# Performance work log

Hardware: AMD Instinct MI355X
Metric: run time of the kernel (lower is better)

The kernel has to match this reference:

```python
import jax, jax.numpy as jnp
import numpy as np

N = 4096
D_MODEL = 512


def setup_inputs() -> dict:
    key = jax.random.key(0)
    ks = jax.random.split(key, 5)
    scale = 1.0 / np.sqrt(D_MODEL)
    return {
        "x": jax.random.normal(ks[0], (N, D_MODEL), dtype=jnp.float32),
        "Wq": jax.random.normal(ks[1], (D_MODEL, D_MODEL), dtype=jnp.float32) * scale,
        "Wk": jax.random.normal(ks[2], (D_MODEL, D_MODEL), dtype=jnp.float32) * scale,
        "Wv": jax.random.normal(ks[3], (D_MODEL, D_MODEL), dtype=jnp.float32) * scale,
        "Ws": jax.random.normal(ks[4], (1, D_MODEL), dtype=jnp.float32) * scale,
    }


def reference(x, Wq, Wk, Wv, Ws):
    # x: [N, d]; torch nn.Linear(bias=False) computes x @ W.T
    Q = x @ Wq.T  # [N, d]
    K = x @ Wk.T  # [N, d]
    V = x @ Wv.T  # [N, d]
    sigma = jnp.clip(x @ Ws.T, 0.001, 1.0)  # [N, 1]

    # prior association: Gaussian kernel over |i - j| with per-row sigma
    pos = jnp.arange(sigma.shape[0], dtype=jnp.float32)
    diff = jnp.abs(pos[:, None] - pos[None, :])  # [N, N]
    gaussian = jnp.exp(-0.5 * (diff / sigma) ** 2) / jnp.sqrt(2.0 * jnp.pi * sigma)
    P = gaussian / (gaussian.sum(axis=1, keepdims=True) + 1e-8)

    scale = jnp.sqrt(jnp.float32(x.shape[-1]))
    S = jax.nn.softmax((Q @ K.T) / scale, axis=-1)  # [N, N]
    Z = S @ V  # [N, d]
    return Z, P, S
```

## Files before the change

kernel.cpp:

```cpp
#include <hip/hip_runtime.h>
#include <math.h>

#define N_TOK 4096
#define DM 512

typedef _Float16 f16x8 __attribute__((ext_vector_type(8)));
typedef _Float16 f16x4 __attribute__((ext_vector_type(4)));
typedef float f32x4 __attribute__((ext_vector_type(4)));

__device__ __forceinline__ void async_ld16(const ushort* g, ushort* l) {
  __builtin_amdgcn_global_load_lds(
      (const __attribute__((address_space(1))) void*)g,
      (__attribute__((address_space(3))) void*)l, 16, 0, 0);
}

__global__ __launch_bounds__(256) void pack_sigma(
    const float* __restrict__ x, const float* __restrict__ Wq,
    const float* __restrict__ Wk, const float* __restrict__ Wv,
    const float* __restrict__ Ws, _Float16* __restrict__ x16,
    _Float16* __restrict__ Wc16, float* __restrict__ sg) {
  const int b = blockIdx.x;
  const int t = threadIdx.x;
  if (b < 2048) {
    int i = b * 1024 + t * 4;
    float4 v = *(const float4*)&x[i];
    f16x4 o;
    o.x = (_Float16)v.x; o.y = (_Float16)v.y;
    o.z = (_Float16)v.z; o.w = (_Float16)v.w;
    *(f16x4*)&x16[i] = o;
    int col = (t * 4) & 511;
    float4 w = *(const float4*)&Ws[col];
    float p = v.x * w.x + v.y * w.y + v.z * w.z + v.w * w.w;
    __shared__ float red[256];
    red[t] = p;
    __syncthreads();
    int lt = t & 127;
    for (int off = 64; off > 0; off >>= 1) {
      if (lt < off) red[t] += red[t + off];
      __syncthreads();
    }
    if (lt == 0) {
      float s = red[t];
      sg[2 * b + (t >> 7)] = fminf(fmaxf(s, 0.001f), 1.0f);
    }
  } else {
    int e = (b - 2048) * 1024 + t * 4;
    const float* src;
    int le = e & (DM * DM - 1);
    if (e < DM * DM) src = Wq + le;
    else if (e < 2 * DM * DM) src = Wk + le;
    else src = Wv + le;
    float4 v = *(const float4*)src;
    f16x4 o;
    o.x = (_Float16)v.x; o.y = (_Float16)v.y;
    o.z = (_Float16)v.z; o.w = (_Float16)v.w;
    *(f16x4*)&Wc16[e] = o;
  }
}

template <int EPI>
__global__ __launch_bounds__(256) void mfma_f16(
    const _Float16* __restrict__ A, int lda, const _Float16* __restrict__ B,
    int ldb, int K, float scale, float* __restrict__ Cf, int ldc,
    _Float16* __restrict__ D0, _Float16* __restrict__ D1,
    _Float16* __restrict__ D2, float* __restrict__ Part) {
  __shared__ _Float16 lds[2 * 128 * 32];
  _Float16* Ah = lds;
  _Float16* Bh = lds + 128 * 32;

  const int t = threadIdx.x;
  const int w = t >> 6, L = t & 63;
  const int wm = (w >> 1) * 64, wn = (w & 1) * 64;
  const int row = L & 15, quad = L >> 4;
  const int bm = blockIdx.y * 128, bn = blockIdx.x * 128;
  const int kbase = blockIdx.z * K;

  f32x4 acc[4][4] = {{}};

  const int c0 = t, c1 = t + 256;
  const int r0 = c0 >> 2, o0 = (c0 & 3) * 8;
  const int r1 = r0 + 64;

  const ushort* ga0 = (const ushort*)(A + (size_t)(bm + r0) * lda + kbase + o0);
  const ushort* ga1 = (const ushort*)(A + (size_t)(bm + r1) * lda + kbase + o0);
  const ushort* gb0 = (const ushort*)(B + (size_t)(bn + r0) * ldb + kbase + o0);
  const ushort* gb1 = (const ushort*)(B + (size_t)(bn + r1) * ldb + kbase + o0);

  for (int k0 = 0; k0 < K; k0 += 32) {
    async_ld16(ga0, (ushort*)(Ah + c0 * 8));
    async_ld16(ga1, (ushort*)(Ah + c1 * 8));
    async_ld16(gb0, (ushort*)(Bh + c0 * 8));
    async_ld16(gb1, (ushort*)(Bh + c1 * 8));
    ga0 += 32; ga1 += 32; gb0 += 32; gb1 += 32;
    __syncthreads();

    f16x8 a0[4], b0[4];
#pragma unroll
    for (int i = 0; i < 4; ++i)
      a0[i] = *(const f16x8*)&Ah[(wm + i * 16 + row) * 32 + quad * 8];
#pragma unroll
    for (int j = 0; j < 4; ++j)
      b0[j] = *(const f16x8*)&Bh[(wn + j * 16 + row) * 32 + quad * 8];
#pragma unroll
    for (int i = 0; i < 4; ++i)
#pragma unroll
      for (int j = 0; j < 4; ++j)
        acc[i][j] = __builtin_amdgcn_mfma_f32_16x16x32_f16(a0[i], b0[j],
                                                           acc[i][j], 0, 0, 0);
    __syncthreads();
  }

  if (EPI == 1) {
    const int region = bn >> 9;
    _Float16* D = (region == 0) ? D0 : ((region == 1) ? D1 : D2);
#pragma unroll
    for (int i = 0; i < 4; ++i)
#pragma unroll
      for (int j = 0; j < 4; ++j)
#pragma unroll
        for (int r = 0; r < 4; ++r) {
          int gr = bm + wm + i * 16 + quad * 4 + r;
          int nn = (bn & 511) + wn + j * 16 + row;
          D[(size_t)gr * 512 + nn] = (_Float16)acc[i][j][r];
        }
  } else if (EPI == 3) {
#pragma unroll
    for (int i = 0; i < 4; ++i)
#pragma unroll
      for (int j = 0; j < 4; ++j)
#pragma unroll
        for (int r = 0; r < 4; ++r) {
          int gr = bm + wm + i * 16 + quad * 4 + r;
          int gc = bn + wn + j * 16 + row;
          D0[(size_t)gr * ldc + gc] = (_Float16)(acc[i][j][r] * scale);
        }
  } else {
    const int z = blockIdx.z;
    float* dst = (z == 0) ? Cf : (Part + (size_t)(z - 1) * 2097152);
#pragma unroll
    for (int i = 0; i < 4; ++i)
#pragma unroll
      for (int j = 0; j < 4; ++j)
#pragma unroll
        for (int r = 0; r < 4; ++r) {
          int gr = bm + wm + i * 16 + quad * 4 + r;
          int gc = bn + wn + j * 16 + row;
          dst[(size_t)gr * ldc + gc] = acc[i][j][r] * scale;
        }
  }
}

__global__ __launch_bounds__(256) void transpose16(
    const _Float16* __restrict__ V16, _Float16* __restrict__ VT) {
  __shared__ _Float16 T[32][34];
  const int t = threadIdx.x;
  const int r = t >> 3, c4 = (t & 7) * 4;
  f16x4 v = *(const f16x4*)&V16[(size_t)(blockIdx.y * 32 + r) * 512 +
                                blockIdx.x * 32 + c4];
  T[r][c4] = v.x; T[r][c4 + 1] = v.y; T[r][c4 + 2] = v.z; T[r][c4 + 3] = v.w;
  __syncthreads();
  f16x4 o;
  o.x = T[c4][r]; o.y = T[c4 + 1][r]; o.z = T[c4 + 2][r]; o.w = T[c4 + 3][r];
  *(f16x4*)&VT[(size_t)(blockIdx.x * 32 + r) * 4096 + blockIdx.y * 32 + c4] = o;
}

__global__ __launch_bounds__(256) void softmax_kernel(
    _Float16* __restrict__ Sc, float* __restrict__ S) {
  __shared__ float red[256];
  const int t = threadIdx.x;
  _Float16* Srow16 = Sc + (size_t)blockIdx.x * N_TOK;
  float* Srow = S + (size_t)blockIdx.x * N_TOK;
  float f[16];
  float m = -INFINITY;
#pragma unroll
  for (int r = 0; r < 4; ++r) {
    f16x4 h = *(const f16x4*)&Srow16[r * 1024 + t * 4];
    f[r * 4 + 0] = (float)h.x; f[r * 4 + 1] = (float)h.y;
    f[r * 4 + 2] = (float)h.z; f[r * 4 + 3] = (float)h.w;
    m = fmaxf(m, fmaxf(fmaxf(f[r * 4], f[r * 4 + 1]),
                       fmaxf(f[r * 4 + 2], f[r * 4 + 3])));
  }
  red[t] = m;
  __syncthreads();
  for (int off = 128; off > 0; off >>= 1) {
    if (t < off) red[t] = fmaxf(red[t], red[t + off]);
    __syncthreads();
  }
  m = red[0];
  __syncthreads();
  float sum = 0.f;
#pragma unroll
  for (int i = 0; i < 16; ++i) {
    f[i] = __expf(f[i] - m);
    sum += f[i];
  }
  red[t] = sum;
  __syncthreads();
  for (int off = 128; off > 0; off >>= 1) {
    if (t < off) red[t] += red[t + off];
    __syncthreads();
  }
  const float inv = 1.0f / red[0];
#pragma unroll
  for (int r = 0; r < 4; ++r) {
    float4 o;
    o.x = f[r * 4 + 0] * inv; o.y = f[r * 4 + 1] * inv;
    o.z = f[r * 4 + 2] * inv; o.w = f[r * 4 + 3] * inv;
    *(float4*)&Srow[r * 1024 + t * 4] = o;
    f16x4 h;
    h.x = (_Float16)o.x; h.y = (_Float16)o.y;
    h.z = (_Float16)o.z; h.w = (_Float16)o.w;
    *(f16x4*)&Srow16[r * 1024 + t * 4] = h;
  }
}

__global__ __launch_bounds__(256) void tail_kernel(
    const float* __restrict__ sigma, float* __restrict__ P,
    float* __restrict__ Z, const float* __restrict__ Part) {
  const int t = threadIdx.x;
  if (blockIdx.x >= 4096) {
    int i = (blockIdx.x - 4096) * 1024 + t * 4;
    float4 z = *(const float4*)&Z[i];
    float4 a = *(const float4*)&Part[i];
    float4 b = *(const float4*)&Part[2097152 + i];
    float4 c = *(const float4*)&Part[2 * 2097152 + i];
    z.x += a.x + b.x + c.x;
    z.y += a.y + b.y + c.y;
    z.z += a.z + b.z + c.z;
    z.w += a.w + b.w + c.w;
    *(float4*)&Z[i] = z;
    return;
  }
  __shared__ float red[256];
  const int i = blockIdx.x;
  const float sg = sigma[i];
  const float inv2 = -0.5f / (sg * sg);
  const float c = rsqrtf(6.283185307179586f * sg);
  float4 g[4];
  float sum = 0.f;
#pragma unroll
  for (int r = 0; r < 4; ++r) {
    int j = r * 1024 + t * 4;
    float d0 = (float)(i - j);
    float d1 = (float)(i - j - 1);
    float d2 = (float)(i - j - 2);
    float d3 = (float)(i - j - 3);
    g[r].x = __expf(inv2 * d0 * d0) * c;
    g[r].y = __expf(inv2 * d1 * d1) * c;
    g[r].z = __expf(inv2 * d2 * d2) * c;
    g[r].w = __expf(inv2 * d3 * d3) * c;
    sum += g[r].x + g[r].y + g[r].z + g[r].w;
  }
  red[t] = sum;
  __syncthreads();
  for (int off = 128; off > 0; off >>= 1) {
    if (t < off) red[t] += red[t + off];
    __syncthreads();
  }
  const float inv = 1.0f / (red[0] + 1e-8f);
  float* Prow = P + (size_t)i * N_TOK;
#pragma unroll
  for (int r = 0; r < 4; ++r) {
    g[r].x *= inv; g[r].y *= inv; g[r].z *= inv; g[r].w *= inv;
    *(float4*)&Prow[r * 1024 + t * 4] = g[r];
  }
}

extern "C" void kernel_launch(void* const* d_in, const int* in_sizes, int n_in,
                              void* d_out, int out_size, void* d_ws,
                              size_t ws_size, hipStream_t stream) {
  const float* x = (const float*)d_in[0];
  const float* Wq = (const float*)d_in[1];
  const float* Wk = (const float*)d_in[2];
  const float* Wv = (const float*)d_in[3];
  const float* Ws = (const float*)d_in[4];

  float* out = (float*)d_out;
  float* Z = out;
  float* Pout = Z + (size_t)N_TOK * DM;
  float* S = Pout + (size_t)N_TOK * N_TOK;

  const size_t E = (size_t)N_TOK * DM;
  _Float16* Q16 = (_Float16*)Pout;
  _Float16* K16 = Q16 + E;
  _Float16* V16 = K16 + E;
  _Float16* VT16 = V16 + E;
  _Float16* Sc16 = VT16 + E;

  _Float16* x16 = (_Float16*)d_ws;
  _Float16* Wc16 = x16 + E;
  float* sg = (float*)(Wc16 + 3 * DM * DM);
  float* Part = sg + 4096;

  const dim3 blk(256);

  pack_sigma<<<2816, blk, 0, stream>>>(x, Wq, Wk, Wv, Ws, x16, Wc16, sg);

  mfma_f16<1><<<dim3(12, 32), blk, 0, stream>>>(
      x16, DM, Wc16, DM, DM, 1.0f, nullptr, 0, Q16, K16, V16, nullptr);

  transpose16<<<dim3(16, 128), blk, 0, stream>>>(V16, VT16);

  mfma_f16<3><<<dim3(32, 32), blk, 0, stream>>>(
      Q16, DM, K16, DM, DM, 1.0f / sqrtf((float)DM), nullptr, N_TOK, Sc16,
      nullptr, nullptr, nullptr);

  softmax_kernel<<<N_TOK, blk, 0, stream>>>(Sc16, S);

  mfma_f16<2><<<dim3(4, 32, 4), blk, 0, stream>>>(
      Sc16, N_TOK, VT16, N_TOK, N_TOK / 4, 1.0f, Z, DM, nullptr, nullptr,
      nullptr, Part);

  tail_kernel<<<4096 + 2048, blk, 0, stream>>>(sg, Pout, Z, Part);
}
```

Before: 261.1 us.

## Replace split-K SV GEMM with full-K kernel fused with prior-P generation

Removes the split-K S@V GEMM, its partial-sum buffers and the reduction tail. A dedicated 64x128-tile kernel now computes Z over the full K range, and the Gaussian prior P rows are computed by extra blocks of the same launch. The fp16 staging buffers move from the P output region into the workspace when it is large enough, which is what lets P be written concurrently with the GEMM. The cost is only 256 GEMM blocks, each running a long K loop with a single LDS buffer, which can underuse the CUs. When the workspace is too small it falls back to two separate launches.

```diff
diff --git a/kernel.cpp b/kernel.cpp
--- a/kernel.cpp
+++ b/kernel.cpp
@@ -123,7 +123,7 @@
           int nn = (bn & 511) + wn + j * 16 + row;
           D[(size_t)gr * 512 + nn] = (_Float16)acc[i][j][r];
         }
-  } else if (EPI == 3) {
+  } else {
 #pragma unroll
     for (int i = 0; i < 4; ++i)
 #pragma unroll
@@ -133,19 +133,6 @@
           int gr = bm + wm + i * 16 + quad * 4 + r;
           int gc = bn + wn + j * 16 + row;
           D0[(size_t)gr * ldc + gc] = (_Float16)(acc[i][j][r] * scale);
-        }
-  } else {
-    const int z = blockIdx.z;
-    float* dst = (z == 0) ? Cf : (Part + (size_t)(z - 1) * 2097152);
-#pragma unroll
-    for (int i = 0; i < 4; ++i)
-#pragma unroll
-      for (int j = 0; j < 4; ++j)
-#pragma unroll
-        for (int r = 0; r < 4; ++r) {
-          int gr = bm + wm + i * 16 + quad * 4 + r;
-          int gc = bn + wn + j * 16 + row;
-          dst[(size_t)gr * ldc + gc] = acc[i][j][r] * scale;
         }
   }
 }
@@ -214,24 +201,116 @@
   }
 }
 
-__global__ __launch_bounds__(256) void tail_kernel(
-    const float* __restrict__ sigma, float* __restrict__ P,
-    float* __restrict__ Z, const float* __restrict__ Part) {
-  const int t = threadIdx.x;
-  if (blockIdx.x >= 4096) {
-    int i = (blockIdx.x - 4096) * 1024 + t * 4;
-    float4 z = *(const float4*)&Z[i];
-    float4 a = *(const float4*)&Part[i];
-    float4 b = *(const float4*)&Part[2097152 + i];
-    float4 c = *(const float4*)&Part[2 * 2097152 + i];
-    z.x += a.x + b.x + c.x;
-    z.y += a.y + b.y + c.y;
-    z.z += a.z + b.z + c.z;
-    z.w += a.w + b.w + c.w;
-    *(float4*)&Z[i] = z;
+template <int FUSE_P>
+__global__ __launch_bounds__(256) void sv_kernel(
+    const _Float16* __restrict__ A,
+    const _Float16* __restrict__ B,
+    float* __restrict__ C,
+    const float* __restrict__ sigma, float* __restrict__ P) {
+  __shared__ _Float16 lds[2 * 64 * 32 + 2 * 128 * 32];
+  const int t = threadIdx.x;
+
+  if (FUSE_P && blockIdx.y >= 64) {
+    float* red = (float*)lds;
+    const int i = (blockIdx.y - 64) * 4 + blockIdx.x;
+    const float sg = sigma[i];
+    const float inv2 = -0.5f / (sg * sg);
+    const float c = rsqrtf(6.283185307179586f * sg);
+    float4 g[4];
+    float sum = 0.f;
+#pragma unroll
+    for (int r = 0; r < 4; ++r) {
+      int j = r * 1024 + t * 4;
+      float d0 = (float)(i - j);
+      float d1 = d0 - 1.f;
+      float d2 = d0 - 2.f;
+      float d3 = d0 - 3.f;
+      g[r].x = __expf(inv2 * d0 * d0) * c;
+      g[r].y = __expf(inv2 * d1 * d1) * c;
+      g[r].z = __expf(inv2 * d2 * d2) * c;
+      g[r].w = __expf(inv2 * d3 * d3) * c;
+      sum += g[r].x + g[r].y + g[r].z + g[r].w;
+    }
+    red[t] = sum;
+    __syncthreads();
+    for (int off = 128; off > 0; off >>= 1) {
+      if (t < off) red[t] += red[t + off];
+      __syncthreads();
+    }
+    const float inv = 1.0f / (red[0] + 1e-8f);
+    float* Prow = P + (size_t)i * N_TOK;
+#pragma unroll
+    for (int r = 0; r < 4; ++r) {
+      g[r].x *= inv; g[r].y *= inv; g[r].z *= inv; g[r].w *= inv;
+      *(float4*)&Prow[r * 1024 + t * 4] = g[r];
+    }
     return;
   }
+
+  _Float16* Ah = lds;
+  _Float16* Bh = lds + 2 * 64 * 32;
+
+  const int w = t >> 6, L = t & 63;
+  const int wm = (w >> 1) * 32, wn = (w & 1) * 64;
+  const int row = L & 15, quad = L >> 4;
+  const int bm = blockIdx.y * 64, bn = blockIdx.x * 128;
+
+  f32x4 acc[2][4] = {{}};
+
+  const int rA = t >> 2, oA = (t & 3) * 8;
+  const ushort* ga = (const ushort*)(A + (size_t)(bm + rA) * N_TOK + oA);
+  const ushort* gb0 = (const ushort*)(B + (size_t)(bn + rA) * N_TOK + oA);
+  const ushort* gb1 = (const ushort*)(B + (size_t)(bn + rA + 64) * N_TOK + oA);
+
+  for (int k0 = 0; k0 < N_TOK; k0 += 64) {
+    async_ld16(ga, (ushort*)(Ah + t * 8));
+    async_ld16(ga + 32, (ushort*)(Ah + 2048 + t * 8));
+    async_ld16(gb0, (ushort*)(Bh + t * 8));
+    async_ld16(gb1, (ushort*)(Bh + (t + 256) * 8));
+    async_ld16(gb0 + 32, (ushort*)(Bh + 4096 + t * 8));
+    async_ld16(gb1 + 32, (ushort*)(Bh + 4096 + (t + 256) * 8));
+    ga += 64; gb0 += 64; gb1 += 64;
+    __syncthreads();
+
+    f16x8 a0[2][2], b0[2][4];
+#pragma unroll
+    for (int kk = 0; kk < 2; ++kk) {
+#pragma unroll
+      for (int i = 0; i < 2; ++i)
+        a0[kk][i] =
+            *(const f16x8*)&Ah[kk * 2048 + (wm + i * 16 + row) * 32 + quad * 8];
+#pragma unroll
+      for (int j = 0; j < 4; ++j)
+        b0[kk][j] =
+            *(const f16x8*)&Bh[kk * 4096 + (wn + j * 16 + row) * 32 + quad * 8];
+    }
+#pragma unroll
+    for (int kk = 0; kk < 2; ++kk)
+#pragma unroll
+      for (int i = 0; i < 2; ++i)
+#pragma unroll
+        for (int j = 0; j < 4; ++j)
+          acc[i][j] = __builtin_amdgcn_mfma_f32_16x16x32_f16(
+              a0[kk][i], b0[kk][j], acc[i][j], 0, 0, 0);
+    __syncthreads();
+  }
+
+#pragma unroll
+  for (int i = 0; i < 2; ++i)
+#pragma unroll
+    for (int j = 0; j < 4; ++j)
+#pragma unroll
+      for (int r = 0; r < 4; ++r) {
+        int gr = bm + wm + i * 16 + quad * 4 + r;
+        int gc = bn + wn + j * 16 + row;
+        C[(size_t)gr * 512 + gc] = acc[i][j][r];
+      }
+}
+
+__global__ __launch_bounds__(256) void tailP(const float* __restrict__ sigma,
+                                             float* __restrict__ P) {
   __shared__ float red[256];
+  const int t = threadIdx.x;
   const int i = blockIdx.x;
   const float sg = sigma[i];
   const float inv2 = -0.5f / (sg * sg);
@@ -242,9 +321,9 @@
   for (int r = 0; r < 4; ++r) {
     int j = r * 1024 + t * 4;
     float d0 = (float)(i - j);
-    float d1 = (float)(i - j - 1);
-    float d2 = (float)(i - j - 2);
-    float d3 = (float)(i - j - 3);
+    float d1 = d0 - 1.f;
+    float d2 = d0 - 2.f;
+    float d3 = d0 - 3.f;
     g[r].x = __expf(inv2 * d0 * d0) * c;
     g[r].y = __expf(inv2 * d1 * d1) * c;
     g[r].z = __expf(inv2 * d2 * d2) * c;
@@ -281,17 +360,22 @@
   float* S = Pout + (size_t)N_TOK * N_TOK;
 
   const size_t E = (size_t)N_TOK * DM;
-  _Float16* Q16 = (_Float16*)Pout;
+
+  _Float16* x16 = (_Float16*)d_ws;
+  _Float16* Wc16 = x16 + E;
+  float* sg = (float*)(Wc16 + 3 * DM * DM);
+  _Float16* stage = (_Float16*)(sg + 4096);
+
+  const size_t stage_bytes = (4 * E + (size_t)N_TOK * N_TOK) * sizeof(_Float16);
+  const size_t base_bytes = (size_t)((char*)stage - (char*)d_ws);
+  const bool ws_ok = ws_size >= base_bytes + stage_bytes;
+
+  _Float16* Q16 = ws_ok ? stage : (_Float16*)Pout;
   _Float16* K16 = Q16 + E;
   _Float16* V16 = K16 + E;
   _Float16* VT16 = V16 + E;
   _Float16* Sc16 = VT16 + E;
 
-  _Float16* x16 = (_Float16*)d_ws;
-  _Float16* Wc16 = x16 + E;
-  float* sg = (float*)(Wc16 + 3 * DM * DM);
-  float* Part = sg + 4096;
-
   const dim3 blk(256);
 
   pack_sigma<<<2816, blk, 0, stream>>>(x, Wq, Wk, Wv, Ws, x16, Wc16, sg);
@@ -307,9 +391,12 @@
 
   softmax_kernel<<<N_TOK, blk, 0, stream>>>(Sc16, S);
 
-  mfma_f16<2><<<dim3(4, 32, 4), blk, 0, stream>>>(
-      Sc16, N_TOK, VT16, N_TOK, N_TOK / 4, 1.0f, Z, DM, nullptr, nullptr,
-      nullptr, Part);
-
-  tail_kernel<<<4096 + 2048, blk, 0, stream>>>(sg, Pout, Z, Part);
-}
+  if (ws_ok) {
+    sv_kernel<1><<<dim3(4, 64 + 1024), blk, 0, stream>>>(Sc16, VT16, Z, sg,
+                                                         Pout);
+  } else {
+    sv_kernel<0><<<dim3(4, 64), blk, 0, stream>>>(Sc16, VT16, Z, nullptr,
+                                                  nullptr);
+    tailP<<<N_TOK, blk, 0, stream>>>(sg, Pout);
+  }
+}
```

Result: slower. 267.1 us (+2.3%).
